# Optimization experiments

Measured on AMD Instinct MI355X. Metric: run time of the kernel, lower is better.

The kernel has to match this reference:

```python
import jax, jax.numpy as jnp
import numpy as np

N_TILES, NX = 6, 96
IN_C, HID_C = 128, 256
BATCH = 4


def _build_neighbors(n_tiles=N_TILES, nx=NX):
    # 4-connectivity on each tile with periodic wrap (fixed cubed-sphere-style
    # grid graph; preserves the gather/mean access pattern of build_dgl_graph).
    i, j = np.meshgrid(np.arange(nx), np.arange(nx), indexing='ij')
    idx = lambda ii, jj: (ii % nx) * nx + (jj % nx)
    per_tile = np.stack([idx(i - 1, j), idx(i + 1, j), idx(i, j - 1), idx(i, j + 1)],
                        axis=-1).reshape(nx * nx, 4)
    offsets = (np.arange(n_tiles) * nx * nx)[:, None, None]
    return (per_tile[None] + offsets).reshape(-1, 4).astype(np.int32)


def setup_inputs() -> dict:
    key = jax.random.key(0)
    ks = jax.random.split(key, 6)
    s = lambda fan_in: 1.0 / np.sqrt(fan_in)
    return {
        'x': jax.random.normal(ks[0], (BATCH, N_TILES, NX, NX, IN_C), jnp.float32),
        'neighbors': jnp.asarray(_build_neighbors()),
        'W_self1': jax.random.normal(ks[1], (IN_C, HID_C), jnp.float32) * s(IN_C),
        'W_neigh1': jax.random.normal(ks[2], (IN_C, HID_C), jnp.float32) * s(IN_C),
        'b1': jnp.zeros((HID_C,), jnp.float32),
        'W_self2': jax.random.normal(ks[3], (HID_C, HID_C), jnp.float32) * s(HID_C),
        'W_neigh2': jax.random.normal(ks[4], (HID_C, HID_C), jnp.float32) * s(HID_C),
        'b2': jnp.zeros((HID_C,), jnp.float32),
    }


def _sage_conv(h, neighbors, W_self, W_neigh, b):
    # h: [B, N, C]; neighbors: [N, 4] -> mean-aggregated SAGEConv
    h_neigh = jnp.mean(h[:, neighbors], axis=2)  # [B, N, 4, C] -> [B, N, C]
    return jnp.einsum('bnc,cd->bnd', h, W_self) + \
           jnp.einsum('bnc,cd->bnd', h_neigh, W_neigh) + b


def reference(x, neighbors, W_self1, W_neigh1, b1, W_self2, W_neigh2, b2):
    B, T, X, Y, C = x.shape
    h = x.reshape(B, T * X * Y, C)                      # flatten sphere -> nodes
    h = jax.nn.relu(_sage_conv(h, neighbors, W_self1, W_neigh1, b1))
    h = jax.nn.relu(_sage_conv(h, neighbors, W_self2, W_neigh2, b2))
    return h.reshape(B, T, X, Y, -1)
```

## Files before the change

kernel.cpp:

```cpp
#include <hip/hip_runtime.h>
#include <stdint.h>

typedef __attribute__((ext_vector_type(8))) short short8;
typedef __attribute__((ext_vector_type(4))) float f32x4;

#define NNODES 55296
#define DOUT 256

#define WAIT_VM(N) asm volatile("s_waitcnt vmcnt(" #N ")" ::: "memory")
#define WAIT_LGKM0 asm volatile("s_waitcnt lgkmcnt(0)" ::: "memory")
#define SOFT_FENCE asm volatile("" ::: "memory")

__device__ __forceinline__ float bf2f(unsigned short h) {
    union { unsigned u; float f; } x; x.u = ((unsigned)h) << 16; return x.f;
}
__device__ __forceinline__ unsigned short f2bf(float f) {
    union { float f; unsigned u; } x; x.f = f;
    return (unsigned short)((x.u + 0x7fffu + ((x.u >> 16) & 1u)) >> 16);
}

__device__ __forceinline__ void storev(float* p, float v) { *p = v; }
__device__ __forceinline__ void storev(unsigned short* p, float v) { *p = f2bf(v); }

__device__ __forceinline__ void dma16(const void* g, void* l) {
    __builtin_amdgcn_global_load_lds(
        reinterpret_cast<const unsigned int __attribute__((address_space(1)))*>((uintptr_t)g),
        reinterpret_cast<unsigned int __attribute__((address_space(3)))*>((uintptr_t)l),
        16, 0, 0);
}

__device__ __forceinline__ short8 frag_self(const float* p) {
    float4 a = *(const float4*)p, b = *(const float4*)(p + 4);
    union { short8 s; unsigned short u[8]; } r;
    r.u[0] = f2bf(a.x); r.u[1] = f2bf(a.y); r.u[2] = f2bf(a.z); r.u[3] = f2bf(a.w);
    r.u[4] = f2bf(b.x); r.u[5] = f2bf(b.y); r.u[6] = f2bf(b.z); r.u[7] = f2bf(b.w);
    return r.s;
}
__device__ __forceinline__ short8 frag_self(const unsigned short* p) {
    return *(const short8*)p;
}
__device__ __forceinline__ void acc8(const float* p, float* o) {
    float4 a = *(const float4*)p, b = *(const float4*)(p + 4);
    o[0] += a.x; o[1] += a.y; o[2] += a.z; o[3] += a.w;
    o[4] += b.x; o[5] += b.y; o[6] += b.z; o[7] += b.w;
}
__device__ __forceinline__ void acc8(const unsigned short* p, float* o) {
    uint4 v = *(const uint4*)p;
    const unsigned short* u = (const unsigned short*)&v;
#pragma unroll
    for (int i = 0; i < 8; ++i) o[i] += bf2f(u[i]);
}
template <typename TIN>
__device__ __forceinline__ short8 frag_mean4(const TIN* p0, const TIN* p1,
                                             const TIN* p2, const TIN* p3) {
    float s[8] = {0.f, 0.f, 0.f, 0.f, 0.f, 0.f, 0.f, 0.f};
    acc8(p0, s); acc8(p1, s); acc8(p2, s); acc8(p3, s);
    union { short8 s8; unsigned short u[8]; } r;
#pragma unroll
    for (int i = 0; i < 8; ++i) r.u[i] = f2bf(s[i] * 0.25f);
    return r.s8;
}

__global__ void build_wt(const float* __restrict__ Ws,
                         const float* __restrict__ Wn,
                         unsigned short* __restrict__ Wt, int C) {
    int K2 = 2 * C;
    int idx = blockIdx.x * 256 + threadIdx.x;
    if (idx >= 256 * K2) return;
    int d = idx / K2;
    int k = idx - d * K2;
    float v = (k < C) ? Ws[(size_t)k * DOUT + d] : Wn[(size_t)(k - C) * DOUT + d];
    Wt[idx] = f2bf(v);
}

__global__ __launch_bounds__(256) void mean_xb(const float* __restrict__ x,
                                               const int* __restrict__ nbr,
                                               unsigned short* __restrict__ xm) {
    const int idx = blockIdx.x * 256 + threadIdx.x;
    const int node = idx >> 4;
    const int ch = (idx & 15) * 8;
    const int b = node / NNODES;
    const int n = node - b * NNODES;
    const size_t bbase = (size_t)b * NNODES;
    const int4 nb = *(const int4*)(nbr + (size_t)n * 4);
    const float* ps = x + (size_t)node * 128 + ch;
    union { uint4 v; unsigned short u[8]; } rs, rm;
    float4 a0 = *(const float4*)ps, a1 = *(const float4*)(ps + 4);
    rs.u[0] = f2bf(a0.x); rs.u[1] = f2bf(a0.y); rs.u[2] = f2bf(a0.z); rs.u[3] = f2bf(a0.w);
    rs.u[4] = f2bf(a1.x); rs.u[5] = f2bf(a1.y); rs.u[6] = f2bf(a1.z); rs.u[7] = f2bf(a1.w);
    float s[8] = {0.f, 0.f, 0.f, 0.f, 0.f, 0.f, 0.f, 0.f};
    acc8(x + (bbase + nb.x) * 128 + ch, s);
    acc8(x + (bbase + nb.y) * 128 + ch, s);
    acc8(x + (bbase + nb.z) * 128 + ch, s);
    acc8(x + (bbase + nb.w) * 128 + ch, s);
#pragma unroll
    for (int i = 0; i < 8; ++i) rm.u[i] = f2bf(s[i] * 0.25f);
    *(uint4*)(xm + (size_t)node * 256 + ch) = rs.v;
    *(uint4*)(xm + (size_t)node * 256 + 128 + ch) = rm.v;
}

template <int C, typename TIN>
__global__ __launch_bounds__(256) void mean_pass(const TIN* __restrict__ hin,
                                                 const int* __restrict__ nbr,
                                                 unsigned short* __restrict__ hm) {
    constexpr int CPL = C / 8;
    const int idx = blockIdx.x * 256 + threadIdx.x;
    const int node = idx / CPL;
    const int ch = (idx - node * CPL) * 8;
    const int b = node / NNODES;
    const int n = node - b * NNODES;
    const size_t bbase = (size_t)b * NNODES;
    const int4 nb = *(const int4*)(nbr + (size_t)n * 4);
    float s[8] = {0.f, 0.f, 0.f, 0.f, 0.f, 0.f, 0.f, 0.f};
    acc8(hin + (bbase + nb.x) * (size_t)C + ch, s);
    acc8(hin + (bbase + nb.y) * (size_t)C + ch, s);
    acc8(hin + (bbase + nb.z) * (size_t)C + ch, s);
    acc8(hin + (bbase + nb.w) * (size_t)C + ch, s);
    union { uint4 v; unsigned short u[8]; } r;
#pragma unroll
    for (int i = 0; i < 8; ++i) r.u[i] = f2bf(s[i] * 0.25f);
    *(uint4*)(hm + (size_t)node * C + ch) = r.v;
}

template <int NK, typename TOUT>
__global__ __launch_bounds__(256) void sage_v12(
    const unsigned short* __restrict__ h1p,
    const unsigned short* __restrict__ hmp,
    const unsigned short* __restrict__ Wt,
    const float* __restrict__ bias,
    TOUT* __restrict__ out,
    int nwg) {
    extern __shared__ char lds[];
    constexpr int WB = NK * 64;
    const int tid = threadIdx.x;
    const int bid = blockIdx.x;
    const int wk = (bid & 7) * (nwg >> 3) + (bid >> 3);
    const int yg = wk & 1;
    const int rb = wk >> 1;
    const int gcol0 = yg * 128;
    const int rowbase = rb * 128;

    const int l = tid & 63, w = tid >> 6;
    const int lr = l & 15, lg = l >> 4;
    const int rowg = w >> 1;
    const int colb = (w & 1) * 64;

    const char* wsrc = (const char*)Wt + (size_t)gcol0 * WB;

    auto stageW = [&](int s) {
#pragma unroll
        for (int i = 0; i < 8; ++i) {
            int o = w * 1024 + i * 4096 + l * 16;
            int col = o >> 8, kq = o & 255;
            dma16(wsrc + (unsigned)(col * WB + s * 256 + (kq ^ ((col & 7) << 4))),
                  lds + w * 1024 + i * 4096);
        }
    };
    auto issueA = [&](int p) {
        const char* base = (NK == 16 && p >= 8) ? (const char*)hmp : (const char*)h1p;
        const unsigned kb = (unsigned)(p & 7) * 64;
        char* ring = lds + 32768 + (p % 3) * 8192;
#pragma unroll
        for (int i = 0; i < 2; ++i) {
            const int cj = w + i * 4;
            const int row = rowbase + cj * 16 + lr;
            dma16(base + ((unsigned)row * 512 + kb + (unsigned)(lg << 4)),
                  ring + cj * 1024);
        }
    };

    issueA(0); stageW(0); issueA(1);

    f32x4 acc[4][4];
#pragma unroll
    for (int m = 0; m < 4; ++m)
#pragma unroll
        for (int j = 0; j < 4; ++j) acc[m][j] = (f32x4){0.f, 0.f, 0.f, 0.f};

    const int abase = rowg * 4096 + lg * 256 + lr * 16;
    const int wbase = (colb + lr) << 8;

#pragma unroll
    for (int kk = 0; kk < NK; ++kk) {
        if (kk == NK - 1) { WAIT_VM(0); } else { WAIT_VM(2); }
        __builtin_amdgcn_s_barrier();
        SOFT_FENCE;

        const int bufo = 32768 + (kk % 3) * 8192;
        short8 af[4];
#pragma unroll
        for (int m = 0; m < 4; ++m)
            af[m] = *(const short8*)(lds + bufo + abase + m * 1024);

#pragma unroll
        for (int j = 0; j < 4; ++j) {
            const short8 wf = *(const short8*)(
                lds + wbase + (j << 12) +
                ((((kk & 3) << 6) | (lg << 4)) ^ ((lr & 7) << 4)));
#pragma unroll
            for (int m = 0; m < 4; ++m)
                acc[m][j] = __builtin_amdgcn_mfma_f32_16x16x32_bf16(wf, af[m], acc[m][j], 0, 0, 0);
        }

        if ((kk & 3) == 3 && kk < NK - 1) {
            WAIT_LGKM0;
            __builtin_amdgcn_sched_barrier(0);
            __builtin_amdgcn_s_barrier();
            stageW((kk >> 2) + 1);
        }
        if (kk + 2 < NK) issueA(kk + 2);
        SOFT_FENCE;
    }

#pragma unroll
    for (int m = 0; m < 4; ++m) {
        const int row = rowbase + rowg * 64 + m * 16 + lr;
#pragma unroll
        for (int j = 0; j < 4; ++j) {
            const int gcol = gcol0 + colb + j * 16 + lg * 4;
            const float4 bv = *(const float4*)(bias + gcol);
            float o0 = fmaxf(acc[m][j][0] + bv.x, 0.f);
            float o1 = fmaxf(acc[m][j][1] + bv.y, 0.f);
            float o2 = fmaxf(acc[m][j][2] + bv.z, 0.f);
            float o3 = fmaxf(acc[m][j][3] + bv.w, 0.f);
            if constexpr (sizeof(TOUT) == 4) {
                float4 o = {o0, o1, o2, o3};
                *(float4*)((float*)out + (size_t)row * 256 + gcol) = o;
            } else {
                union { unsigned short u[4]; uint2 v; } pk;
                pk.u[0] = f2bf(o0); pk.u[1] = f2bf(o1);
                pk.u[2] = f2bf(o2); pk.u[3] = f2bf(o3);
                *(uint2*)((unsigned short*)out + (size_t)row * 256 + gcol) = pk.v;
            }
        }
    }
}

template <int C, typename TIN, typename TOUT>
__global__ __launch_bounds__(512, 2) void sage_v3(
    const TIN* __restrict__ hin, const int* __restrict__ nbr,
    const unsigned short* __restrict__ Wt, const float* __restrict__ bias,
    TOUT* __restrict__ out) {
    constexpr int K2 = 2 * C;
    constexpr int ROWB = K2 * 2;
    constexpr int LCOLS = 131072 / ROWB;
    constexpr int CG = LCOLS / 128;
    constexpr int RG = 8 / CG;
    extern __shared__ char Bs[];

    const int tid = threadIdx.x;
    const int gcol0 = blockIdx.y * LCOLS;
    {
        const char* src = (const char*)(Wt + (size_t)gcol0 * K2);
#pragma unroll
        for (int i = 0; i < 16; ++i) {
            int byt = (i * 512 + tid) * 16;
            uint4 v = *(const uint4*)(src + byt);
            int c = byt / ROWB;
            *(uint4*)(Bs + (byt ^ ((c & 7) << 4))) = v;
        }
    }
    __syncthreads();

    const int l = tid & 63;
    const int w = tid >> 6;
    const int rowg = w / CG;
    const int colb = (w % CG) * 128;
    const int lr = l & 15, lg = l >> 4;

    const int rowbase = blockIdx.x * (RG * 64) + rowg * 64;
    const int bb = rowbase / NNODES;
    const int n0 = rowbase - bb * NNODES;
    const size_t bbase = (size_t)bb * NNODES;

    unsigned soff[4], noff[4][4];
#pragma unroll
    for (int m = 0; m < 4; ++m) {
        int r = m * 16 + lr;
        soff[m] = (unsigned)(((rowbase + r) * (size_t)C + lg * 8) * sizeof(TIN));
        int4 nb = *(const int4*)(nbr + (size_t)(n0 + r) * 4);
        noff[m][0] = (unsigned)(((bbase + nb.x) * C + lg * 8) * sizeof(TIN));
        noff[m][1] = (unsigned)(((bbase + nb.y) * C + lg * 8) * sizeof(TIN));
        noff[m][2] = (unsigned)(((bbase + nb.z) * C + lg * 8) * sizeof(TIN));
        noff[m][3] = (unsigned)(((bbase + nb.w) * C + lg * 8) * sizeof(TIN));
    }
    const char* hb = (const char*)hin;

    f32x4 acc[4][8];
#pragma unroll
    for (int m = 0; m < 4; ++m)
#pragma unroll
        for (int j = 0; j < 8; ++j) acc[m][j] = (f32x4){0.f, 0.f, 0.f, 0.f};

#pragma unroll
    for (int kk = 0; kk < K2 / 32; ++kk) {
        const int k0 = kk * 32;
        short8 a[4];
        if (k0 < C) {
            const unsigned kb = k0 * sizeof(TIN);
#pragma unroll
            for (int m = 0; m < 4; ++m)
                a[m] = frag_self((const TIN*)(hb + soff[m] + kb));
        } else {
            const unsigned kb = (k0 - C) * sizeof(TIN);
#pragma unroll
            for (int m = 0; m < 4; ++m)
                a[m] = frag_mean4((const TIN*)(hb + noff[m][0] + kb),
                                  (const TIN*)(hb + noff[m][1] + kb),
                                  (const TIN*)(hb + noff[m][2] + kb),
                                  (const TIN*)(hb + noff[m][3] + kb));
        }
#pragma unroll
        for (int j = 0; j < 8; ++j) {
            const int c = colb + j * 16 + lr;
            const short8 bf = *(const short8*)(
                Bs + ((c * ROWB + (k0 + lg * 8) * 2) ^ ((l & 7) << 4)));
#pragma unroll
            for (int m = 0; m < 4; ++m)
                acc[m][j] = __builtin_amdgcn_mfma_f32_16x16x32_bf16(a[m], bf, acc[m][j], 0, 0, 0);
        }
    }

#pragma unroll
    for (int j = 0; j < 8; ++j) {
        const int gcol = gcol0 + colb + j * 16 + lr;
        const float bv = bias[gcol];
#pragma unroll
        for (int m = 0; m < 4; ++m) {
#pragma unroll
            for (int r = 0; r < 4; ++r) {
                const int row = rowbase + m * 16 + lg * 4 + r;
                storev(out + (size_t)row * DOUT + gcol, fmaxf(acc[m][j][r] + bv, 0.f));
            }
        }
    }
}

extern "C" void kernel_launch(void* const* d_in, const int* in_sizes, int n_in,
                              void* d_out, int out_size, void* d_ws, size_t ws_size,
                              hipStream_t stream) {
    const float* x = (const float*)d_in[0];
    const int* nbr = (const int*)d_in[1];
    const float* Ws1 = (const float*)d_in[2];
    const float* Wn1 = (const float*)d_in[3];
    const float* b1 = (const float*)d_in[4];
    const float* Ws2 = (const float*)d_in[5];
    const float* Wn2 = (const float*)d_in[6];
    const float* b2 = (const float*)d_in[7];
    float* out = (float*)d_out;

    const int B = in_sizes[0] / (NNODES * 128);
    const int M = B * NNODES;

    char* ws = (char*)d_ws;
    const size_t h1_bytes = (size_t)M * DOUT * 2;
    const size_t hm_bytes = (size_t)M * DOUT * 2;
    const size_t need = h1_bytes + hm_bytes + 131072 + 262144;

    if (ws_size >= need) {
        unsigned short* h1 = (unsigned short*)ws;
        unsigned short* xm = (unsigned short*)(ws + h1_bytes);
        unsigned short* Wt1 = (unsigned short*)(ws + h1_bytes + hm_bytes);
        unsigned short* Wt2 = Wt1 + 256 * 256;

        build_wt<<<256, 256, 0, stream>>>(Ws1, Wn1, Wt1, 128);
        build_wt<<<512, 256, 0, stream>>>(Ws2, Wn2, Wt2, 256);

        hipFuncSetAttribute((const void*)sage_v12<8, unsigned short>,
                            hipFuncAttributeMaxDynamicSharedMemorySize, 57344);
        hipFuncSetAttribute((const void*)sage_v12<16, float>,
                            hipFuncAttributeMaxDynamicSharedMemorySize, 57344);

        const int nwg = (M / 128) * 2;

        mean_xb<<<M / 16, 256, 0, stream>>>(x, nbr, xm);
        sage_v12<8, unsigned short>
            <<<nwg, 256, 57344, stream>>>(xm, xm, Wt1, b1, h1, nwg);
        mean_pass<256, unsigned short><<<M * 32 / 256, 256, 0, stream>>>(h1, nbr, xm);
        sage_v12<16, float>
            <<<nwg, 256, 57344, stream>>>(h1, xm, Wt2, b2, out, nwg);
    } else {
        unsigned short* h1 = (unsigned short*)ws;
        unsigned short* Wt1 = (unsigned short*)(ws + h1_bytes);
        unsigned short* Wt2 = Wt1 + 256 * 256;

        build_wt<<<256, 256, 0, stream>>>(Ws1, Wn1, Wt1, 128);
        build_wt<<<512, 256, 0, stream>>>(Ws2, Wn2, Wt2, 256);

        hipFuncSetAttribute((const void*)sage_v3<128, float, unsigned short>,
                            hipFuncAttributeMaxDynamicSharedMemorySize, 131072);
        hipFuncSetAttribute((const void*)sage_v3<256, unsigned short, float>,
                            hipFuncAttributeMaxDynamicSharedMemorySize, 131072);

        sage_v3<128, float, unsigned short>
            <<<dim3(M / 256, 1), 512, 131072, stream>>>(x, nbr, Wt1, b1, h1);
        sage_v3<256, unsigned short, float>
            <<<dim3(M / 512, 2), 512, 131072, stream>>>(h1, nbr, Wt2, b2, out);
    }
}
```

Baseline: 351.6 us.

## Double-buffer weight tiles and deepen A-ring to four stages in SAGE GEMM

Weight staging changes from one 32KB block reloaded every four k-steps behind an extra lgkm wait and barrier to two 16KB double buffers, each refilled every two k-steps. The A-tile ring goes from three to four slots with three loads in flight, and all DMA issues now happen right after the per-step barrier instead of after the MFMAs. The aim is to remove the mid-loop stall on weight reloads and hide more global latency. LDS use per block rises from 56KB to 64KB, which may lower occupancy, and the vmcnt wait counts become more intricate.

```diff
diff --git a/kernel.cpp b/kernel.cpp
--- a/kernel.cpp
+++ b/kernel.cpp
@@ -8,7 +8,6 @@
 #define DOUT 256
 
 #define WAIT_VM(N) asm volatile("s_waitcnt vmcnt(" #N ")" ::: "memory")
-#define WAIT_LGKM0 asm volatile("s_waitcnt lgkmcnt(0)" ::: "memory")
 #define SOFT_FENCE asm volatile("" ::: "memory")
 
 __device__ __forceinline__ float bf2f(unsigned short h) {
@@ -123,7 +122,7 @@
 }
 
 template <int NK, typename TOUT>
-__global__ __launch_bounds__(256) void sage_v12(
+__global__ __launch_bounds__(256) void sage_v13(
     const unsigned short* __restrict__ h1p,
     const unsigned short* __restrict__ hmp,
     const unsigned short* __restrict__ Wt,
@@ -147,19 +146,20 @@
 
     const char* wsrc = (const char*)Wt + (size_t)gcol0 * WB;
 
-    auto stageW = [&](int s) {
-#pragma unroll
-        for (int i = 0; i < 8; ++i) {
+    auto stageW = [&](int q) {
+        char* wb = lds + ((q & 1) << 14);
+#pragma unroll
+        for (int i = 0; i < 4; ++i) {
             int o = w * 1024 + i * 4096 + l * 16;
-            int col = o >> 8, kq = o & 255;
-            dma16(wsrc + (unsigned)(col * WB + s * 256 + (kq ^ ((col & 7) << 4))),
-                  lds + w * 1024 + i * 4096);
+            int col = o >> 7, kq = o & 127;
+            dma16(wsrc + (unsigned)(col * WB + q * 128 + (kq ^ ((col & 7) << 4))),
+                  wb + o);
         }
     };
     auto issueA = [&](int p) {
         const char* base = (NK == 16 && p >= 8) ? (const char*)hmp : (const char*)h1p;
         const unsigned kb = (unsigned)(p & 7) * 64;
-        char* ring = lds + 32768 + (p % 3) * 8192;
+        char* ring = lds + 32768 + (p & 3) * 8192;
 #pragma unroll
         for (int i = 0; i < 2; ++i) {
             const int cj = w + i * 4;
@@ -169,7 +169,7 @@
         }
     };
 
-    issueA(0); stageW(0); issueA(1);
+    stageW(0); issueA(0); issueA(1); issueA(2);
 
     f32x4 acc[4][4];
 #pragma unroll
@@ -178,37 +178,43 @@
         for (int j = 0; j < 4; ++j) acc[m][j] = (f32x4){0.f, 0.f, 0.f, 0.f};
 
     const int abase = rowg * 4096 + lg * 256 + lr * 16;
-    const int wbase = (colb + lr) << 8;
 
 #pragma unroll
     for (int kk = 0; kk < NK; ++kk) {
-        if (kk == NK - 1) { WAIT_VM(0); } else { WAIT_VM(2); }
+        int n;
+        if (kk == 0) n = 4;
+        else if (kk & 1) n = ((kk + 1 < NK) ? 6 : 0) + ((kk + 2 < NK) ? 2 : 0);
+        else n = 2 + ((kk + 2 < NK) ? 2 : 0);
+        switch (n) {
+            case 0: WAIT_VM(0); break;
+            case 2: WAIT_VM(2); break;
+            case 4: WAIT_VM(4); break;
+            case 6: WAIT_VM(6); break;
+            default: WAIT_VM(8); break;
+        }
         __builtin_amdgcn_s_barrier();
         SOFT_FENCE;
 
-        const int bufo = 32768 + (kk % 3) * 8192;
+        if (((kk & 1) == 0) && (kk + 2 < NK)) stageW((kk + 2) >> 1);
+        if (kk + 3 < NK) issueA(kk + 3);
+
+        const int bufo = 32768 + (kk & 3) * 8192;
         short8 af[4];
 #pragma unroll
         for (int m = 0; m < 4; ++m)
             af[m] = *(const short8*)(lds + bufo + abase + m * 1024);
 
+        char* wbuf = lds + (((kk >> 1) & 1) << 14);
+        const int kq0 = ((kk & 1) << 6) | (lg << 4);
 #pragma unroll
         for (int j = 0; j < 4; ++j) {
+            const int col = colb + j * 16 + lr;
             const short8 wf = *(const short8*)(
-                lds + wbase + (j << 12) +
-                ((((kk & 3) << 6) | (lg << 4)) ^ ((lr & 7) << 4)));
+                wbuf + (col << 7) + (kq0 ^ ((lr & 7) << 4)));
 #pragma unroll
             for (int m = 0; m < 4; ++m)
                 acc[m][j] = __builtin_amdgcn_mfma_f32_16x16x32_bf16(wf, af[m], acc[m][j], 0, 0, 0);
         }
-
-        if ((kk & 3) == 3 && kk < NK - 1) {
-            WAIT_LGKM0;
-            __builtin_amdgcn_sched_barrier(0);
-            __builtin_amdgcn_s_barrier();
-            stageW((kk >> 2) + 1);
-        }
-        if (kk + 2 < NK) issueA(kk + 2);
         SOFT_FENCE;
     }
 
@@ -366,19 +372,19 @@
         build_wt<<<256, 256, 0, stream>>>(Ws1, Wn1, Wt1, 128);
         build_wt<<<512, 256, 0, stream>>>(Ws2, Wn2, Wt2, 256);
 
-        hipFuncSetAttribute((const void*)sage_v12<8, unsigned short>,
-                            hipFuncAttributeMaxDynamicSharedMemorySize, 57344);
-        hipFuncSetAttribute((const void*)sage_v12<16, float>,
-                            hipFuncAttributeMaxDynamicSharedMemorySize, 57344);
+        hipFuncSetAttribute((const void*)sage_v13<8, unsigned short>,
+                            hipFuncAttributeMaxDynamicSharedMemorySize, 65536);
+        hipFuncSetAttribute((const void*)sage_v13<16, float>,
+                            hipFuncAttributeMaxDynamicSharedMemorySize, 65536);
 
         const int nwg = (M / 128) * 2;
 
         mean_xb<<<M / 16, 256, 0, stream>>>(x, nbr, xm);
-        sage_v12<8, unsigned short>
-            <<<nwg, 256, 57344, stream>>>(xm, xm, Wt1, b1, h1, nwg);
+        sage_v13<8, unsigned short>
+            <<<nwg, 256, 65536, stream>>>(xm, xm, Wt1, b1, h1, nwg);
         mean_pass<256, unsigned short><<<M * 32 / 256, 256, 0, stream>>>(h1, nbr, xm);
-        sage_v12<16, float>
-            <<<nwg, 256, 57344, stream>>>(h1, xm, Wt2, b2, out, nwg);
+        sage_v13<16, float>
+            <<<nwg, 256, 65536, stream>>>(h1, xm, Wt2, b2, out, nwg);
     } else {
         unsigned short* h1 = (unsigned short*)ws;
         unsigned short* Wt1 = (unsigned short*)(ws + h1_bytes);
```

Result: no change. 346.1 us (-1.5%).
